# Kernel tuning notes

Hardware: AMD Instinct MI355X
Metric: run time of the kernel (lower is better)

The kernel has to match this reference:

```python
import jax, jax.numpy as jnp
import numpy as np

SINKHORN_ITERS = 5
EPS = 1e-12  # torch F.normalize eps


def _l2norm(x):
    n = jnp.sqrt(jnp.sum(x * x, axis=-1, keepdims=True))
    return x / jnp.maximum(n, EPS)


def setup_inputs() -> dict:
    key = jax.random.key(0)
    k1, k2, k3, k4 = jax.random.split(key, 4)
    B, Nd, Ns, D, Dm = 8, 2048, 2048, 1024, 256
    drone_nodes = jax.random.normal(k1, (B, Nd, D), dtype=jnp.float32)
    sat_nodes = jax.random.normal(k2, (B, Ns, D), dtype=jnp.float32)
    # match_proj parameters (nn.Linear(d_model, match_dim))
    lim = 1.0 / np.sqrt(D)
    W = jax.random.uniform(k3, (D, Dm), minval=-lim, maxval=lim, dtype=jnp.float32)
    b = jax.random.uniform(k4, (Dm,), minval=-lim, maxval=lim, dtype=jnp.float32)
    return {"drone_nodes": drone_nodes, "sat_nodes": sat_nodes, "W": W, "b": b}


def reference(drone_nodes, sat_nodes, W, b):
    # project + L2-normalize each node embedding
    d = _l2norm(drone_nodes @ W + b)   # [B, Nd, Dm]
    s = _l2norm(sat_nodes @ W + b)     # [B, Ns, Dm]
    M0 = jnp.einsum('bnd,bmd->bnm', d, s)  # [B, Nd, Ns] cosine similarities
    M = M0
    for _ in range(SINKHORN_ITERS):
        M = M - jax.nn.logsumexp(M, axis=2, keepdims=True)
        M = M - jax.nn.logsumexp(M, axis=1, keepdims=True)
    assignment = jnp.exp(M)
    denom = min(d.shape[1], s.shape[1])
    match_score = jnp.sum(assignment * M0, axis=(1, 2)) / denom  # [B]
    return (assignment, match_score)
```

## Files before the change

### kernel.cpp

```cpp
#include <hip/hip_runtime.h>
#include <math.h>

#define BATCH 8
#define NNODE 2048
#define DIN   1024
#define DM    256
#define ROWS_TOTAL (BATCH * NNODE)

#define LOG2E 1.4426950408889634f
#define Q127  0.011359803471566641f
#define INV127 0.007874015748031496f

typedef unsigned short u16;
typedef __attribute__((ext_vector_type(8))) short short8;
typedef __attribute__((ext_vector_type(4))) float f32x4;

__device__ __forceinline__ u16 f2b(float f) {
    union { float f; unsigned u; } v; v.f = f;
    unsigned r = v.u + 0x7fffu + ((v.u >> 16) & 1u);
    return (u16)(r >> 16);
}
__device__ __forceinline__ float dqi(unsigned wd, int k) {
    return (float)((int)(wd << ((3 - k) * 8)) >> 24);
}

__global__ __launch_bounds__(256) void cvgm_prep_w(
    const float* __restrict__ W, u16* __restrict__ Wt)
{
    __shared__ float t[32][33];
    const int tx = threadIdx.x & 31, ty = threadIdx.x >> 5;
    const int k0 = blockIdx.x * 32, c0 = blockIdx.y * 32;
    #pragma unroll
    for (int r = 0; r < 4; ++r) {
        const int kl = ty * 4 + r;
        t[kl][tx] = W[(size_t)(k0 + kl) * DM + c0 + tx];
    }
    __syncthreads();
    #pragma unroll
    for (int r = 0; r < 4; ++r) {
        const int cl = ty * 4 + r;
        Wt[(size_t)(c0 + cl) * DIN + k0 + tx] = f2b(t[tx][cl]);
    }
}

__global__ __launch_bounds__(512) void cvgm_proj_mfma(
    const float* __restrict__ Xd, const float* __restrict__ Xs,
    const u16* __restrict__ Wt, const float* __restrict__ bias,
    u16* __restrict__ Pd, u16* __restrict__ Ps)
{
    __shared__ u16 As[64 * 64];
    __shared__ u16 Bs[256 * 64];
    __shared__ float rsum[4][64];

    const float* X = blockIdx.y ? Xs : Xd;
    u16* P = blockIdx.y ? Ps : Pd;

    const int tid = threadIdx.x;
    const int lane = tid & 63, wid = tid >> 6;
    const int wr = wid >> 2, wc = wid & 3;
    const int l15 = lane & 15, l4 = lane >> 4;
    const int row0 = blockIdx.x * 64;

    f32x4 acc[2][4];
    #pragma unroll
    for (int m = 0; m < 2; ++m)
        #pragma unroll
        for (int n = 0; n < 4; ++n) acc[m][n] = (f32x4){0.f, 0.f, 0.f, 0.f};

    const int arow = tid >> 3, ac = tid & 7;

    for (int k0 = 0; k0 < DIN; k0 += 64) {
        const float* src = X + (size_t)(row0 + arow) * DIN + k0 + ac * 8;
        const float4 x0 = *(const float4*)src;
        const float4 x1 = *(const float4*)(src + 4);
        short8 wb[4];
        #pragma unroll
        for (int it = 0; it < 4; ++it) {
            const int id = it * 512 + tid;
            const int col = id >> 3, cc = id & 7;
            wb[it] = *(const short8*)(Wt + (size_t)col * DIN + k0 + cc * 8);
        }
        __syncthreads();
        short8 ap;
        ap[0]=(short)f2b(x0.x); ap[1]=(short)f2b(x0.y); ap[2]=(short)f2b(x0.z); ap[3]=(short)f2b(x0.w);
        ap[4]=(short)f2b(x1.x); ap[5]=(short)f2b(x1.y); ap[6]=(short)f2b(x1.z); ap[7]=(short)f2b(x1.w);
        *(short8*)(As + (arow * 8 + (ac ^ (arow & 7))) * 8) = ap;
        #pragma unroll
        for (int it = 0; it < 4; ++it) {
            const int id = it * 512 + tid;
            const int col = id >> 3, cc = id & 7;
            *(short8*)(Bs + (col * 8 + (cc ^ (col & 7))) * 8) = wb[it];
        }
        __syncthreads();
        #pragma unroll
        for (int ks = 0; ks < 2; ++ks) {
            const int ch = ks * 4 + l4;
            short8 af[2], bfr[4];
            #pragma unroll
            for (int m = 0; m < 2; ++m) {
                const int row = wr * 32 + m * 16 + l15;
                af[m] = *(const short8*)(As + (row * 8 + (ch ^ (row & 7))) * 8);
            }
            #pragma unroll
            for (int n = 0; n < 4; ++n) {
                const int col = wc * 64 + n * 16 + l15;
                bfr[n] = *(const short8*)(Bs + (col * 8 + (ch ^ (col & 7))) * 8);
            }
            #pragma unroll
            for (int m = 0; m < 2; ++m)
                #pragma unroll
                for (int n = 0; n < 4; ++n)
                    acc[m][n] = __builtin_amdgcn_mfma_f32_16x16x32_bf16(af[m], bfr[n], acc[m][n], 0, 0, 0);
        }
        __syncthreads();
    }

    #pragma unroll
    for (int n = 0; n < 4; ++n) {
        const float bv = bias[wc * 64 + n * 16 + l15];
        #pragma unroll
        for (int m = 0; m < 2; ++m)
            #pragma unroll
            for (int r = 0; r < 4; ++r) acc[m][n][r] += bv;
    }
    #pragma unroll
    for (int m = 0; m < 2; ++m)
        #pragma unroll
        for (int r = 0; r < 4; ++r) {
            float s = 0.f;
            #pragma unroll
            for (int n = 0; n < 4; ++n) s += acc[m][n][r] * acc[m][n][r];
            s += __shfl_xor(s, 1); s += __shfl_xor(s, 2);
            s += __shfl_xor(s, 4); s += __shfl_xor(s, 8);
            if (l15 == 0) rsum[wc][wr * 32 + m * 16 + l4 * 4 + r] = s;
        }
    __syncthreads();
    #pragma unroll
    for (int m = 0; m < 2; ++m)
        #pragma unroll
        for (int r = 0; r < 4; ++r) {
            const int row = wr * 32 + m * 16 + l4 * 4 + r;
            const float tot = rsum[0][row] + rsum[1][row] + rsum[2][row] + rsum[3][row];
            const float inv = 1.0f / fmaxf(sqrtf(tot), 1e-12f);
            #pragma unroll
            for (int n = 0; n < 4; ++n) {
                const int col = wc * 64 + n * 16 + l15;
                P[(size_t)(row0 + row) * DM + col] = f2b(acc[m][n][r] * inv);
            }
        }
}

__global__ __launch_bounds__(256) void cvgm_m0_mfma(
    const u16* __restrict__ Dp, const u16* __restrict__ Sp,
    char* __restrict__ Cq)
{
    __shared__ u16 As[128 * 64];
    __shared__ u16 Bs[128 * 64];

    const int tid = threadIdx.x;
    const int lane = tid & 63, wid = tid >> 6;
    const int wr = wid >> 1, wc = wid & 1;
    const int l15 = lane & 15, l4 = lane >> 4;
    const int bb = blockIdx.z;
    const int i0 = blockIdx.y * 128, j0 = blockIdx.x * 128;
    const u16* Db = Dp + (size_t)bb * NNODE * DM;
    const u16* Sb = Sp + (size_t)bb * NNODE * DM;

    f32x4 acc[4][4];
    #pragma unroll
    for (int m = 0; m < 4; ++m)
        #pragma unroll
        for (int n = 0; n < 4; ++n) acc[m][n] = (f32x4){0.f, 0.f, 0.f, 0.f};

    for (int k0 = 0; k0 < DM; k0 += 64) {
        short8 ra[4], rb[4];
        #pragma unroll
        for (int it = 0; it < 4; ++it) {
            const int id = it * 256 + tid;
            const int row = id >> 3, c = id & 7;
            ra[it] = *(const short8*)(Db + (size_t)(i0 + row) * DM + k0 + c * 8);
            rb[it] = *(const short8*)(Sb + (size_t)(j0 + row) * DM + k0 + c * 8);
        }
        __syncthreads();
        #pragma unroll
        for (int it = 0; it < 4; ++it) {
            const int id = it * 256 + tid;
            const int row = id >> 3, c = id & 7;
            const int sl = row * 8 + (c ^ (row & 7));
            *(short8*)(As + sl * 8) = ra[it];
            *(short8*)(Bs + sl * 8) = rb[it];
        }
        __syncthreads();
        #pragma unroll
        for (int ks = 0; ks < 2; ++ks) {
            const int ch = ks * 4 + l4;
            short8 af[4], bfr[4];
            #pragma unroll
            for (int m = 0; m < 4; ++m) {
                const int row = wr * 64 + m * 16 + l15;
                af[m] = *(const short8*)(As + (row * 8 + (ch ^ (row & 7))) * 8);
            }
            #pragma unroll
            for (int n = 0; n < 4; ++n) {
                const int col = wc * 64 + n * 16 + l15;
                bfr[n] = *(const short8*)(Bs + (col * 8 + (ch ^ (col & 7))) * 8);
            }
            #pragma unroll
            for (int m = 0; m < 4; ++m)
                #pragma unroll
                for (int n = 0; n < 4; ++n)
                    acc[m][n] = __builtin_amdgcn_mfma_f32_16x16x32_bf16(af[m], bfr[n], acc[m][n], 0, 0, 0);
        }
        __syncthreads();
    }

    char* Cqb = Cq + (size_t)bb * NNODE * NNODE;
    #pragma unroll
    for (int m = 0; m < 4; ++m) {
        const int row = i0 + wr * 64 + m * 16 + l4 * 4;
        #pragma unroll
        for (int n = 0; n < 4; ++n) {
            const int col = j0 + wc * 64 + n * 16 + l15;
            #pragma unroll
            for (int r = 0; r < 4; ++r) {
                int q = __float2int_rn(acc[m][n][r] * 127.f);
                q = q > 127 ? 127 : (q < -127 ? -127 : q);
                Cqb[(size_t)(row + r) * NNODE + col] = (char)q;
            }
        }
    }
}

__global__ __launch_bounds__(256) void cvgm_rc(
    const char* __restrict__ Mq, const float* __restrict__ v2,
    float* __restrict__ u2, float* __restrict__ ps)
{
    __shared__ float cps[4][NNODE];

    const int tid = threadIdx.x;
    const int lane = tid & 63, w = tid >> 6;
    const int b = blockIdx.y, chunk = blockIdx.x;
    const size_t row0 = ((size_t)b << 11) + chunk * 16;
    const float* v2b = v2 + (b << 11);

    float wv[32];
    #pragma unroll
    for (int s = 0; s < 2; ++s)
        #pragma unroll
        for (int k = 0; k < 4; ++k) {
            const float4 vv = *(const float4*)(v2b + s * 1024 + lane * 16 + k * 4);
            wv[s*16+k*4+0] = exp2f(-vv.x);
            wv[s*16+k*4+1] = exp2f(-vv.y);
            wv[s*16+k*4+2] = exp2f(-vv.z);
            wv[s*16+k*4+3] = exp2f(-vv.w);
        }

    const char* gb = Mq + row0 * NNODE + lane * 16;

    float sc[32];
    #pragma unroll
    for (int k = 0; k < 32; ++k) sc[k] = 0.f;

    #pragma unroll
    for (int rr = 0; rr < 4; ++rr) {
        const char* rsrc = gb + (size_t)(w * 4 + rr) * NNODE;
        const int4 d0 = *(const int4*)(rsrc);
        const int4 d1 = *(const int4*)(rsrc + 1024);
        const unsigned qd[8] = {(unsigned)d0.x, (unsigned)d0.y, (unsigned)d0.z, (unsigned)d0.w,
                                (unsigned)d1.x, (unsigned)d1.y, (unsigned)d1.z, (unsigned)d1.w};
        float p[32];
        #pragma unroll
        for (int q = 0; q < 8; ++q)
            #pragma unroll
            for (int k = 0; k < 4; ++k)
                p[q * 4 + k] = exp2f(dqi(qd[q], k) * Q127);
        float s = 0.f;
        #pragma unroll
        for (int k = 0; k < 32; ++k) s = fmaf(p[k], wv[k], s);
        #pragma unroll
        for (int off = 1; off < 64; off <<= 1) s += __shfl_xor(s, off);
        const float ur = __log2f(s);
        if (lane == 0) u2[row0 + w * 4 + rr] = ur;
        const float eu = exp2f(-ur);
        #pragma unroll
        for (int k = 0; k < 32; ++k) sc[k] = fmaf(p[k], eu, sc[k]);
    }

    #pragma unroll
    for (int s = 0; s < 2; ++s)
        #pragma unroll
        for (int k = 0; k < 4; ++k)
            *(float4*)(&cps[w][s * 1024 + lane * 16 + k * 4]) =
                make_float4(sc[s*16+k*4+0], sc[s*16+k*4+1], sc[s*16+k*4+2], sc[s*16+k*4+3]);
    __syncthreads();

    const int j = tid * 8;
    float4 a0 = *(const float4*)(&cps[0][j]), a1 = *(const float4*)(&cps[0][j + 4]);
    #pragma unroll
    for (int ww = 1; ww < 4; ++ww) {
        const float4 b0 = *(const float4*)(&cps[ww][j]);
        const float4 b1 = *(const float4*)(&cps[ww][j + 4]);
        a0.x += b0.x; a0.y += b0.y; a0.z += b0.z; a0.w += b0.w;
        a1.x += b1.x; a1.y += b1.y; a1.z += b1.z; a1.w += b1.w;
    }
    float* dst = ps + ((size_t)(b * 128 + chunk)) * NNODE + j;
    *(float4*)dst = a0;
    *(float4*)(dst + 4) = a1;
}

__global__ __launch_bounds__(256) void cvgm_merge(
    const float* __restrict__ ps, float* __restrict__ v2)
{
    const int idx = blockIdx.x * 256 + threadIdx.x;
    const int b = idx >> 11, j = idx & 2047;
    float s = 0.f;
    #pragma unroll 8
    for (int c = 0; c < 128; ++c) s += ps[(size_t)(b * 128 + c) * NNODE + j];
    v2[idx] = __log2f(s);
}

__global__ __launch_bounds__(128) void cvgm_final(
    const char* __restrict__ Mq, const float* __restrict__ u2,
    const float* __restrict__ v2, float* __restrict__ out,
    float* __restrict__ spart)
{
    const int row = (blockIdx.y << 11) + blockIdx.x;
    const int t = threadIdx.x;
    const float ui = u2[row];
    const float* v2b = v2 + (blockIdx.y << 11);

    float vl[16];
    #pragma unroll
    for (int k = 0; k < 4; ++k)
        *(float4*)(vl + k * 4) = *(const float4*)(v2b + t * 16 + k * 4);

    const int4 d = *(const int4*)(Mq + (size_t)row * NNODE + t * 16);
    const unsigned qd[4] = {(unsigned)d.x, (unsigned)d.y, (unsigned)d.z, (unsigned)d.w};

    float a[16], acc = 0.f;
    #pragma unroll
    for (int q = 0; q < 4; ++q)
        #pragma unroll
        for (int k = 0; k < 4; ++k) {
            const float xq = dqi(qd[q], k);
            const float e = exp2f(fmaf(xq, Q127, -(ui + vl[q * 4 + k])));
            a[q * 4 + k] = e;
            acc = fmaf(e, xq, acc);
        }
    float* drow = out + (size_t)row * NNODE + t * 16;
    #pragma unroll
    for (int k = 0; k < 4; ++k)
        *(float4*)(drow + k * 4) = make_float4(a[k*4+0], a[k*4+1], a[k*4+2], a[k*4+3]);

    acc *= INV127;
    #pragma unroll
    for (int off = 1; off < 64; off <<= 1) acc += __shfl_xor(acc, off);
    __shared__ float sh[2];
    if ((t & 63) == 0) sh[t >> 6] = acc;
    __syncthreads();
    if (t == 0) spart[row] = sh[0] + sh[1];
}

__global__ __launch_bounds__(256) void cvgm_score(
    const float* __restrict__ spart, float* __restrict__ score)
{
    const int b = blockIdx.x;
    float acc = 0.f;
    for (int t = threadIdx.x; t < NNODE; t += 256) acc += spart[(b << 11) + t];
    #pragma unroll
    for (int off = 1; off < 64; off <<= 1) acc += __shfl_xor(acc, off);
    __shared__ float sh[4];
    if ((threadIdx.x & 63) == 0) sh[threadIdx.x >> 6] = acc;
    __syncthreads();
    if (threadIdx.x == 0) score[b] = (sh[0] + sh[1] + sh[2] + sh[3]) * (1.0f / 2048.0f);
}

extern "C" void kernel_launch(void* const* d_in, const int* in_sizes, int n_in,
                              void* d_out, int out_size, void* d_ws, size_t ws_size,
                              hipStream_t stream) {
    (void)in_sizes; (void)n_in; (void)out_size; (void)ws_size;
    const float* drone = (const float*)d_in[0];
    const float* sat   = (const float*)d_in[1];
    const float* W     = (const float*)d_in[2];
    const float* bias  = (const float*)d_in[3];

    float* out   = (float*)d_out;
    float* score = out + (size_t)BATCH * NNODE * NNODE;

    char* ws = (char*)d_ws;
    const size_t SZ_M0Q  = (size_t)BATCH * NNODE * NNODE;
    const size_t SZ_PROJ = (size_t)ROWS_TOTAL * DM * 2;
    const size_t SZ_WT   = (size_t)DM * DIN * 2;
    const size_t SZ_UV   = (size_t)ROWS_TOTAL * 4;
    const size_t SZ_PS   = (size_t)BATCH * 128 * NNODE * 4;

    size_t off = 0;
    char* M0q  = ws + off;            off += SZ_M0Q;
    u16* dproj = (u16*)(ws + off);    off += SZ_PROJ;
    u16* sproj = (u16*)(ws + off);    off += SZ_PROJ;
    u16* Wt    = (u16*)(ws + off);    off += SZ_WT;
    float* u2  = (float*)(ws + off);  off += SZ_UV;
    float* v2  = (float*)(ws + off);  off += SZ_UV;
    float* ps  = (float*)(ws + off);  off += SZ_PS;
    float* spart = (float*)(ws + off);

    hipMemsetAsync(v2, 0, SZ_UV, stream);
    cvgm_prep_w<<<dim3(32, 8), 256, 0, stream>>>(W, Wt);
    cvgm_proj_mfma<<<dim3(256, 2), 512, 0, stream>>>(drone, sat, Wt, bias, dproj, sproj);
    cvgm_m0_mfma<<<dim3(16, 16, 8), 256, 0, stream>>>(dproj, sproj, M0q);

    for (int it = 0; it < 5; ++it) {
        cvgm_rc<<<dim3(128, 8), 256, 0, stream>>>(M0q, v2, u2, ps);
        cvgm_merge<<<ROWS_TOTAL / 256, 256, 0, stream>>>(ps, v2);
    }

    cvgm_final<<<dim3(2048, 8), 128, 0, stream>>>(M0q, u2, v2, out, spart);
    cvgm_score<<<BATCH, 256, 0, stream>>>(spart, score);
}
```

Before: 262.7 us.

## Replace column-partial merge kernel with atomics and use linear-domain scaling factors

```diff
diff --git a/kernel.cpp b/kernel.cpp
--- a/kernel.cpp
+++ b/kernel.cpp
@@ -7,7 +7,6 @@
 #define DM    256
 #define ROWS_TOTAL (BATCH * NNODE)
 
-#define LOG2E 1.4426950408889634f
 #define Q127  0.011359803471566641f
 #define INV127 0.007874015748031496f
 
@@ -25,8 +24,12 @@
 }
 
 __global__ __launch_bounds__(256) void cvgm_prep_w(
-    const float* __restrict__ W, u16* __restrict__ Wt)
-{
+    const float* __restrict__ W, u16* __restrict__ Wt, float* __restrict__ bufs)
+{
+    const int gid = (blockIdx.y * 32 + blockIdx.x) * 256 + threadIdx.x;
+    for (int i = gid; i < 6 * ROWS_TOTAL; i += 65536)
+        bufs[i] = (i < ROWS_TOTAL) ? 1.0f : 0.0f;
+
     __shared__ float t[32][33];
     const int tx = threadIdx.x & 31, ty = threadIdx.x >> 5;
     const int k0 = blockIdx.x * 32, c0 = blockIdx.y * 32;
@@ -231,9 +234,10 @@
     }
 }
 
+template <int FIRST>
 __global__ __launch_bounds__(256) void cvgm_rc(
-    const char* __restrict__ Mq, const float* __restrict__ v2,
-    float* __restrict__ u2, float* __restrict__ ps)
+    const char* __restrict__ Mq, const float* __restrict__ Sin,
+    float* __restrict__ Sout, float* __restrict__ euo)
 {
     __shared__ float cps[4][NNODE];
 
@@ -241,21 +245,25 @@
     const int lane = tid & 63, w = tid >> 6;
     const int b = blockIdx.y, chunk = blockIdx.x;
     const size_t row0 = ((size_t)b << 11) + chunk * 16;
-    const float* v2b = v2 + (b << 11);
+    const char* gb = Mq + row0 * NNODE + lane * 16;
 
     float wv[32];
-    #pragma unroll
-    for (int s = 0; s < 2; ++s)
-        #pragma unroll
-        for (int k = 0; k < 4; ++k) {
-            const float4 vv = *(const float4*)(v2b + s * 1024 + lane * 16 + k * 4);
-            wv[s*16+k*4+0] = exp2f(-vv.x);
-            wv[s*16+k*4+1] = exp2f(-vv.y);
-            wv[s*16+k*4+2] = exp2f(-vv.z);
-            wv[s*16+k*4+3] = exp2f(-vv.w);
-        }
-
-    const char* gb = Mq + row0 * NNODE + lane * 16;
+    if constexpr (FIRST) {
+        #pragma unroll
+        for (int k = 0; k < 32; ++k) wv[k] = 1.f;
+    } else {
+        const float* Sb = Sin + (b << 11);
+        #pragma unroll
+        for (int s = 0; s < 2; ++s)
+            #pragma unroll
+            for (int k = 0; k < 4; ++k) {
+                const float4 vv = *(const float4*)(Sb + s * 1024 + lane * 16 + k * 4);
+                wv[s*16+k*4+0] = 1.0f / vv.x;
+                wv[s*16+k*4+1] = 1.0f / vv.y;
+                wv[s*16+k*4+2] = 1.0f / vv.z;
+                wv[s*16+k*4+3] = 1.0f / vv.w;
+            }
+    }
 
     float sc[32];
     #pragma unroll
@@ -279,9 +287,8 @@
         for (int k = 0; k < 32; ++k) s = fmaf(p[k], wv[k], s);
         #pragma unroll
         for (int off = 1; off < 64; off <<= 1) s += __shfl_xor(s, off);
-        const float ur = __log2f(s);
-        if (lane == 0) u2[row0 + w * 4 + rr] = ur;
-        const float eu = exp2f(-ur);
+        const float eu = 1.0f / s;
+        if (lane == 0) euo[row0 + w * 4 + rr] = eu;
         #pragma unroll
         for (int k = 0; k < 32; ++k) sc[k] = fmaf(p[k], eu, sc[k]);
     }
@@ -303,62 +310,65 @@
         a0.x += b0.x; a0.y += b0.y; a0.z += b0.z; a0.w += b0.w;
         a1.x += b1.x; a1.y += b1.y; a1.z += b1.z; a1.w += b1.w;
     }
-    float* dst = ps + ((size_t)(b * 128 + chunk)) * NNODE + j;
-    *(float4*)dst = a0;
-    *(float4*)(dst + 4) = a1;
-}
-
-__global__ __launch_bounds__(256) void cvgm_merge(
-    const float* __restrict__ ps, float* __restrict__ v2)
-{
-    const int idx = blockIdx.x * 256 + threadIdx.x;
-    const int b = idx >> 11, j = idx & 2047;
-    float s = 0.f;
-    #pragma unroll 8
-    for (int c = 0; c < 128; ++c) s += ps[(size_t)(b * 128 + c) * NNODE + j];
-    v2[idx] = __log2f(s);
-}
-
-__global__ __launch_bounds__(128) void cvgm_final(
-    const char* __restrict__ Mq, const float* __restrict__ u2,
-    const float* __restrict__ v2, float* __restrict__ out,
+    float* dst = Sout + (b << 11) + j;
+    atomicAdd(dst + 0, a0.x); atomicAdd(dst + 1, a0.y);
+    atomicAdd(dst + 2, a0.z); atomicAdd(dst + 3, a0.w);
+    atomicAdd(dst + 4, a1.x); atomicAdd(dst + 5, a1.y);
+    atomicAdd(dst + 6, a1.z); atomicAdd(dst + 7, a1.w);
+}
+
+__global__ __launch_bounds__(256) void cvgm_final(
+    const char* __restrict__ Mq, const float* __restrict__ eui,
+    const float* __restrict__ Scol, float* __restrict__ out,
     float* __restrict__ spart)
 {
-    const int row = (blockIdx.y << 11) + blockIdx.x;
-    const int t = threadIdx.x;
-    const float ui = u2[row];
-    const float* v2b = v2 + (blockIdx.y << 11);
-
-    float vl[16];
-    #pragma unroll
-    for (int k = 0; k < 4; ++k)
-        *(float4*)(vl + k * 4) = *(const float4*)(v2b + t * 16 + k * 4);
-
-    const int4 d = *(const int4*)(Mq + (size_t)row * NNODE + t * 16);
-    const unsigned qd[4] = {(unsigned)d.x, (unsigned)d.y, (unsigned)d.z, (unsigned)d.w};
-
-    float a[16], acc = 0.f;
-    #pragma unroll
-    for (int q = 0; q < 4; ++q)
-        #pragma unroll
-        for (int k = 0; k < 4; ++k) {
-            const float xq = dqi(qd[q], k);
-            const float e = exp2f(fmaf(xq, Q127, -(ui + vl[q * 4 + k])));
-            a[q * 4 + k] = e;
-            acc = fmaf(e, xq, acc);
-        }
-    float* drow = out + (size_t)row * NNODE + t * 16;
-    #pragma unroll
-    for (int k = 0; k < 4; ++k)
-        *(float4*)(drow + k * 4) = make_float4(a[k*4+0], a[k*4+1], a[k*4+2], a[k*4+3]);
-
-    acc *= INV127;
-    #pragma unroll
-    for (int off = 1; off < 64; off <<= 1) acc += __shfl_xor(acc, off);
-    __shared__ float sh[2];
-    if ((t & 63) == 0) sh[t >> 6] = acc;
-    __syncthreads();
-    if (t == 0) spart[row] = sh[0] + sh[1];
+    const int tid = threadIdx.x;
+    const int lane = tid & 63, w = tid >> 6;
+    const int b = blockIdx.y, chunk = blockIdx.x;
+    const size_t row0 = ((size_t)b << 11) + chunk * 16;
+    const char* gb = Mq + row0 * NNODE + lane * 16;
+
+    float wv[32];
+    {
+        const float* Sb = Scol + (b << 11);
+        #pragma unroll
+        for (int s = 0; s < 2; ++s)
+            #pragma unroll
+            for (int k = 0; k < 4; ++k) {
+                const float4 vv = *(const float4*)(Sb + s * 1024 + lane * 16 + k * 4);
+                wv[s*16+k*4+0] = 1.0f / vv.x;
+                wv[s*16+k*4+1] = 1.0f / vv.y;
+                wv[s*16+k*4+2] = 1.0f / vv.z;
+                wv[s*16+k*4+3] = 1.0f / vv.w;
+            }
+    }
+
+    #pragma unroll
+    for (int rr = 0; rr < 4; ++rr) {
+        const size_t row = row0 + w * 4 + rr;
+        const char* rsrc = gb + (size_t)(w * 4 + rr) * NNODE;
+        float* drow = out + row * NNODE + lane * 16;
+        const float eu = eui[row];
+        const int4 d0 = *(const int4*)(rsrc);
+        const int4 d1 = *(const int4*)(rsrc + 1024);
+        const unsigned qd[8] = {(unsigned)d0.x, (unsigned)d0.y, (unsigned)d0.z, (unsigned)d0.w,
+                                (unsigned)d1.x, (unsigned)d1.y, (unsigned)d1.z, (unsigned)d1.w};
+        float acc = 0.f;
+        #pragma unroll
+        for (int q = 0; q < 8; ++q) {
+            float e[4];
+            #pragma unroll
+            for (int k = 0; k < 4; ++k) {
+                const float xq = dqi(qd[q], k);
+                e[k] = exp2f(xq * Q127) * eu * wv[q * 4 + k];
+                acc = fmaf(e[k], xq, acc);
+            }
+            *(float4*)(drow + (q >> 2) * 1024 + (q & 3) * 4) = make_float4(e[0], e[1], e[2], e[3]);
+        }
+        #pragma unroll
+        for (int off = 1; off < 64; off <<= 1) acc += __shfl_xor(acc, off);
+        if (lane == 0) spart[row] = acc * INV127;
+    }
 }
 
 __global__ __launch_bounds__(256) void cvgm_score(
@@ -392,28 +402,25 @@
     const size_t SZ_PROJ = (size_t)ROWS_TOTAL * DM * 2;
     const size_t SZ_WT   = (size_t)DM * DIN * 2;
     const size_t SZ_UV   = (size_t)ROWS_TOTAL * 4;
-    const size_t SZ_PS   = (size_t)BATCH * 128 * NNODE * 4;
 
     size_t off = 0;
     char* M0q  = ws + off;            off += SZ_M0Q;
     u16* dproj = (u16*)(ws + off);    off += SZ_PROJ;
     u16* sproj = (u16*)(ws + off);    off += SZ_PROJ;
     u16* Wt    = (u16*)(ws + off);    off += SZ_WT;
-    float* u2  = (float*)(ws + off);  off += SZ_UV;
-    float* v2  = (float*)(ws + off);  off += SZ_UV;
-    float* ps  = (float*)(ws + off);  off += SZ_PS;
+    float* bufs = (float*)(ws + off); off += 6 * SZ_UV;
+    float* eu   = (float*)(ws + off); off += SZ_UV;
     float* spart = (float*)(ws + off);
 
-    hipMemsetAsync(v2, 0, SZ_UV, stream);
-    cvgm_prep_w<<<dim3(32, 8), 256, 0, stream>>>(W, Wt);
+    cvgm_prep_w<<<dim3(32, 8), 256, 0, stream>>>(W, Wt, bufs);
     cvgm_proj_mfma<<<dim3(256, 2), 512, 0, stream>>>(drone, sat, Wt, bias, dproj, sproj);
     cvgm_m0_mfma<<<dim3(16, 16, 8), 256, 0, stream>>>(dproj, sproj, M0q);
 
-    for (int it = 0; it < 5; ++it) {
-        cvgm_rc<<<dim3(128, 8), 256, 0, stream>>>(M0q, v2, u2, ps);
-        cvgm_merge<<<ROWS_TOTAL / 256, 256, 0, stream>>>(ps, v2);
-    }
-
-    cvgm_final<<<dim3(2048, 8), 128, 0, stream>>>(M0q, u2, v2, out, spart);
+    cvgm_rc<1><<<dim3(128, 8), 256, 0, stream>>>(M0q, bufs, bufs + ROWS_TOTAL, eu);
+    for (int it = 1; it < 5; ++it)
+        cvgm_rc<0><<<dim3(128, 8), 256, 0, stream>>>(
+            M0q, bufs + (size_t)it * ROWS_TOTAL, bufs + (size_t)(it + 1) * ROWS_TOTAL, eu);
+
+    cvgm_final<<<dim3(128, 8), 256, 0, stream>>>(M0q, eu, bufs + 5 * (size_t)ROWS_TOTAL, out, spart);
     cvgm_score<<<BATCH, 256, 0, stream>>>(spart, score);
 }
```

Result: slower. 561.1 us (+113.6%).
